# Kernel optimization log

Measured on AMD Instinct MI355X. Metric: run time of the kernel, lower is better.

The kernel has to match this reference:

```python
import jax, jax.numpy as jnp
import numpy as np


def setup_inputs() -> dict:
    key = jax.random.key(0)
    k1, k2, k3, k4 = jax.random.split(key, 4)
    Nq, Nk, D = 8192, 8192, 256
    xq = jax.random.normal(k1, (Nq, D), dtype=jnp.float32)
    xk = jax.random.normal(k2, (Nk, D), dtype=jnp.float32)
    Wq = jax.random.normal(k3, (D, D), dtype=jnp.float32)
    Wk = jax.random.normal(k4, (D, D), dtype=jnp.float32)
    return {"xq": xq, "xk": xk, "Wq": Wq, "Wk": Wk}


def reference(xq, xk, Wq, Wk):
    # Q: [Nq, D], K: [Nk, D]
    Q = xq @ Wq
    K = xk @ Wk
    # scores: [Nq, Nk], consumed only by row-wise logsumexp
    scores = Q @ K.T
    # energy: -sum_i logsumexp_j(scores[i, j])
    return -jnp.sum(jax.nn.logsumexp(scores, axis=1))
```

## Files before the change

### kernel.cpp

```cpp
#include <hip/hip_runtime.h>

typedef unsigned short ushort_t;
typedef __attribute__((ext_vector_type(8))) __bf16 bf16x8;
typedef __attribute__((ext_vector_type(4))) float f32x4;
typedef __attribute__((ext_vector_type(4))) unsigned int u32x4;
typedef __attribute__((ext_vector_type(8))) unsigned short u16x8;

#define NQ 8192
#define NK 8192
#define DD 256
#define NSPLIT 8
#define SEG (NK / NSPLIT)
#define KBLK 64
#define NT (SEG / KBLK)
#define LOG2E 1.4426950408889634f
#define LN2 0.6931471805599453f

using gptr_t = const __attribute__((address_space(1))) void*;
using lptr_t = __attribute__((address_space(3))) void*;

__device__ __forceinline__ float fexp2(float x) { return __builtin_amdgcn_exp2f(x); }
__device__ __forceinline__ float flog2(float x) { return __builtin_amdgcn_logf(x); }

__device__ __forceinline__ ushort_t f2bf(float f) {
  unsigned int u = __builtin_bit_cast(unsigned int, f);
  unsigned int r = 0x7FFFu + ((u >> 16) & 1u);
  return (ushort_t)((u + r) >> 16);
}

__global__ __launch_bounds__(256) void proj_kernel(
    const float* __restrict__ xq, const float* __restrict__ xk,
    const float* __restrict__ Wq, const float* __restrict__ Wk,
    ushort_t* __restrict__ Qb, ushort_t* __restrict__ Kb) {
  __shared__ __align__(16) char wt_lds[64 * 512];
  const float* X = (blockIdx.y == 0) ? xq : xk;
  const float* W = (blockIdx.y == 0) ? Wq : Wk;
  ushort_t* OUT = (blockIdx.y == 0) ? Qb : Kb;
  const float scale = (blockIdx.y == 0) ? LOG2E : 1.0f;

  const int tid = threadIdx.x;
  const int w = tid >> 6, lane = tid & 63;
  const int g = lane >> 4, c = lane & 15;
  const int rbase = blockIdx.x * 64 + w * 16;
  const int ctbase = blockIdx.z * 4;

  {
    const int n_ = tid & 63;
    const int kb = (tid >> 6) * 2;
    const int nglob = blockIdx.z * 64 + n_;
#pragma unroll
    for (int i = 0; i < 32; ++i) {
      int k = i * 8 + kb;
      float w0 = W[(size_t)k * 256 + nglob];
      float w1 = W[(size_t)(k + 1) * 256 + nglob];
      unsigned int pk = (unsigned int)f2bf(w0) | ((unsigned int)f2bf(w1) << 16);
      int ch = i ^ (n_ & 7);
      *reinterpret_cast<unsigned int*>(&wt_lds[n_ * 512 + ch * 16 + (k & 7) * 2]) = pk;
    }
  }

  bf16x8 a[8];
#pragma unroll
  for (int kk = 0; kk < 8; ++kk) {
    const f32x4* px =
        reinterpret_cast<const f32x4*>(X + (size_t)(rbase + c) * DD + kk * 32 + g * 8);
    f32x4 x0 = px[0], x1 = px[1];
    u16x8 v;
#pragma unroll
    for (int j = 0; j < 4; ++j) { v[j] = f2bf(x0[j]); v[4 + j] = f2bf(x1[j]); }
    a[kk] = __builtin_bit_cast(bf16x8, v);
  }
  __syncthreads();

#pragma unroll
  for (int ct0 = 0; ct0 < 4; ++ct0) {
    const int jrl = ct0 * 16 + c;
    f32x4 acc = {0.f, 0.f, 0.f, 0.f};
#pragma unroll
    for (int kk = 0; kk < 8; ++kk) {
      int ch = (kk * 4 + g) ^ (c & 7);
      bf16x8 b = *reinterpret_cast<const bf16x8*>(&wt_lds[jrl * 512 + ch * 16]);
      acc = __builtin_amdgcn_mfma_f32_16x16x32_bf16(a[kk], b, acc, 0, 0, 0);
    }
    int ct = ctbase + ct0;
#pragma unroll
    for (int r = 0; r < 4; ++r)
      OUT[(size_t)(rbase + g * 4 + r) * DD + ct * 16 + c] = f2bf(acc[r] * scale);
  }
}

__global__ __launch_bounds__(256, 2) void scores_lse_kernel(
    const ushort_t* __restrict__ Qb, const ushort_t* __restrict__ Kb,
    float* __restrict__ pm, float* __restrict__ ps) {
  __shared__ __align__(128) char smem[2][KBLK * 512];
  const int tid = threadIdx.x;
  const int w = tid >> 6, lane = tid & 63;
  const int g = lane >> 4, c = lane & 15;
  const int qw = blockIdx.x * 128 + w * 32;
  const int j0 = blockIdx.y * SEG;

  bf16x8 a[2][8];
#pragma unroll
  for (int rt = 0; rt < 2; ++rt)
#pragma unroll
    for (int kk = 0; kk < 8; ++kk) {
      u32x4 v = *reinterpret_cast<const u32x4*>(
          Qb + (size_t)(qw + rt * 16 + c) * DD + kk * 32 + g * 8);
      a[rt][kk] = __builtin_bit_cast(bf16x8, v);
    }
  asm volatile("s_waitcnt vmcnt(0)" ::: "memory");

  const int c2 = (c >> 2) & 1;
  const int lbase = c * 512 + ((g ^ (c & 3)) << 4);
  const int base_e = lbase + c2 * 64;
  const int base_o = lbase - c2 * 64;

  float m[2][4], s[2][4];
#pragma unroll
  for (int rt = 0; rt < 2; ++rt)
#pragma unroll
    for (int r = 0; r < 4; ++r) { m[rt][r] = -3.4e38f; s[rt][r] = 0.f; }

  f32x4 accA[2][4], accB[2][4];

#define STAGE(buf, t)                                                          \
  do {                                                                         \
    const char* kbase_ = (const char*)(Kb + (size_t)(j0 + (t) * KBLK) * DD);   \
    _Pragma("unroll") for (int i_ = 0; i_ < 8; ++i_) {                         \
      int L_ = (w * 8 + i_) * 64 + lane;                                       \
      int row_ = L_ >> 5, ch_ = L_ & 31;                                       \
      const char* src_ = kbase_ + row_ * 512 + ((ch_ ^ (row_ & 7)) * 16);      \
      char* dst_ = &smem[buf][L_ * 16];                                        \
      __builtin_amdgcn_global_load_lds((gptr_t)src_, (lptr_t)dst_, 16, 0, 0);  \
    }                                                                          \
  } while (0)

#define MFMA_TILE(buf, C)                                                      \
  do {                                                                         \
    const char* se_ = &smem[buf][0] + base_e;                                  \
    const char* so_ = &smem[buf][0] + base_o;                                  \
    _Pragma("unroll") for (int rt_ = 0; rt_ < 2; ++rt_)                        \
    _Pragma("unroll") for (int jt_ = 0; jt_ < 4; ++jt_)                        \
        C[rt_][jt_] = (f32x4){0.f, 0.f, 0.f, 0.f};                             \
    __builtin_amdgcn_s_setprio(1);                                             \
    _Pragma("unroll") for (int kk_ = 0; kk_ < 8; kk_ += 2) {                   \
      _Pragma("unroll") for (int jt_ = 0; jt_ < 4; ++jt_) {                    \
        bf16x8 be_ = *reinterpret_cast<const bf16x8*>(se_ + jt_ * 8192 + kk_ * 64); \
        bf16x8 bo_ = *reinterpret_cast<const bf16x8*>(so_ + jt_ * 8192 + (kk_ + 1) * 64); \
        C[0][jt_] = __builtin_amdgcn_mfma_f32_16x16x32_bf16(a[0][kk_], be_, C[0][jt_], 0, 0, 0); \
        C[1][jt_] = __builtin_amdgcn_mfma_f32_16x16x32_bf16(a[1][kk_], be_, C[1][jt_], 0, 0, 0); \
        C[0][jt_] = __builtin_amdgcn_mfma_f32_16x16x32_bf16(a[0][kk_ + 1], bo_, C[0][jt_], 0, 0, 0); \
        C[1][jt_] = __builtin_amdgcn_mfma_f32_16x16x32_bf16(a[1][kk_ + 1], bo_, C[1][jt_], 0, 0, 0); \
      }                                                                        \
    }                                                                          \
    __builtin_amdgcn_s_setprio(0);                                             \
  } while (0)

#define FOLD(F)                                                                \
  do {                                                                         \
    _Pragma("unroll") for (int rt_ = 0; rt_ < 2; ++rt_)                        \
    _Pragma("unroll") for (int r_ = 0; r_ < 4; ++r_) {                         \
      float v0_ = F[rt_][0][r_], v1_ = F[rt_][1][r_];                          \
      float v2_ = F[rt_][2][r_], v3_ = F[rt_][3][r_];                          \
      float tm_ = fmaxf(fmaxf(v0_, v1_), fmaxf(v2_, v3_));                     \
      float mo_ = m[rt_][r_];                                                  \
      float mn_ = fmaxf(mo_, tm_);                                             \
      float sc_ = fexp2(mo_ - mn_);                                            \
      s[rt_][r_] = s[rt_][r_] * sc_ +                                          \
                   (fexp2(v0_ - mn_) + fexp2(v1_ - mn_) +                      \
                    fexp2(v2_ - mn_) + fexp2(v3_ - mn_));                      \
      m[rt_][r_] = mn_;                                                        \
    }                                                                          \
  } while (0)

  STAGE(0, 0);
  STAGE(1, 1);
  asm volatile("s_waitcnt vmcnt(8)" ::: "memory");
  __builtin_amdgcn_s_barrier();
  MFMA_TILE(0, accA);
  asm volatile("s_waitcnt lgkmcnt(0)" ::: "memory");
  __builtin_amdgcn_s_barrier();

#pragma unroll 1
  for (int tt = 1; tt + 1 < NT; tt += 2) {
    STAGE(0, tt + 1);
    FOLD(accA);
    asm volatile("s_waitcnt vmcnt(8)" ::: "memory");
    __builtin_amdgcn_s_barrier();
    MFMA_TILE(1, accB);
    asm volatile("s_waitcnt lgkmcnt(0)" ::: "memory");
    __builtin_amdgcn_s_barrier();

    STAGE(1, tt + 2);
    FOLD(accB);
    asm volatile("s_waitcnt vmcnt(8)" ::: "memory");
    __builtin_amdgcn_s_barrier();
    MFMA_TILE(0, accA);
    asm volatile("s_waitcnt lgkmcnt(0)" ::: "memory");
    __builtin_amdgcn_s_barrier();
  }

  FOLD(accA);
  asm volatile("s_waitcnt vmcnt(0)" ::: "memory");
  __builtin_amdgcn_s_barrier();
  MFMA_TILE(1, accB);
  FOLD(accB);
#undef STAGE
#undef MFMA_TILE
#undef FOLD

#pragma unroll
  for (int rt = 0; rt < 2; ++rt)
#pragma unroll
    for (int r = 0; r < 4; ++r) {
      float M = m[rt][r], S = s[rt][r];
#pragma unroll
      for (int off = 1; off < 16; off <<= 1) {
        float Mo = __shfl_xor(M, off);
        float So = __shfl_xor(S, off);
        float Mn = fmaxf(M, Mo);
        S = S * fexp2(M - Mn) + So * fexp2(Mo - Mn);
        M = Mn;
      }
      if (c == 0) {
        int row = qw + rt * 16 + g * 4 + r;
        pm[blockIdx.y * NQ + row] = M;
        ps[blockIdx.y * NQ + row] = S;
      }
    }
}

__global__ __launch_bounds__(128) void finalize1_kernel(
    const float* __restrict__ pm, const float* __restrict__ ps,
    float* __restrict__ part) {
  const int tid = threadIdx.x;
  const int row = blockIdx.x * 128 + tid;
  float M = -3.4e38f;
#pragma unroll
  for (int k = 0; k < NSPLIT; ++k) M = fmaxf(M, pm[k * NQ + row]);
  float S = 0.f;
#pragma unroll
  for (int k = 0; k < NSPLIT; ++k) S += ps[k * NQ + row] * fexp2(pm[k * NQ + row] - M);
  float v = LN2 * (M + flog2(S));

  __shared__ float red[128];
  red[tid] = v;
  __syncthreads();
#pragma unroll
  for (int st = 64; st > 0; st >>= 1) {
    if (tid < st) red[tid] += red[tid + st];
    __syncthreads();
  }
  if (tid == 0) part[blockIdx.x] = red[0];
}

__global__ __launch_bounds__(64) void finalize2_kernel(
    const float* __restrict__ part, float* __restrict__ out) {
  const int lane = threadIdx.x;
  float v = part[lane];
#pragma unroll
  for (int off = 1; off < 64; off <<= 1) v += __shfl_xor(v, off);
  if (lane == 0) out[0] = -v;
}

extern "C" void kernel_launch(void* const* d_in, const int* in_sizes, int n_in,
                              void* d_out, int out_size, void* d_ws, size_t ws_size,
                              hipStream_t stream) {
  const float* xq = (const float*)d_in[0];
  const float* xk = (const float*)d_in[1];
  const float* Wq = (const float*)d_in[2];
  const float* Wk = (const float*)d_in[3];

  char* ws = (char*)d_ws;
  ushort_t* Qb = (ushort_t*)(ws);
  ushort_t* Kb = (ushort_t*)(ws + (size_t)NQ * DD * 2);
  float* pm = (float*)(ws + (size_t)(NQ + NK) * DD * 2);
  float* ps = pm + (size_t)NSPLIT * NQ;
  float* part = ps + (size_t)NSPLIT * NQ;

  hipLaunchKernelGGL(proj_kernel, dim3(128, 2, 4), dim3(256), 0, stream,
                     xq, xk, Wq, Wk, Qb, Kb);
  hipLaunchKernelGGL(scores_lse_kernel, dim3(NQ / 128, NSPLIT), dim3(256), 0, stream,
                     Qb, Kb, pm, ps);
  hipLaunchKernelGGL(finalize1_kernel, dim3(64), dim3(128), 0, stream, pm, ps, part);
  hipLaunchKernelGGL(finalize2_kernel, dim3(1), dim3(64), 0, stream, part, (float*)d_out);
}
```

Before: 62.21 us.

## Interleave K-tile prefetch with per-column-tile LDS reads and MFMA phases

Restructures the main loop from a two-accumulator ping-pong, where FOLD overlapped with the next tile's MFMAs, into a single accumulator with four phases per K tile. Each phase reads one column sub-tile from LDS, issues a quarter of the next tile's global-to-LDS prefetch, then runs its MFMAs. The aim is to spread memory traffic more evenly across compute and cut register use. In exchange it adds many more barriers per tile and the softmax fold no longer overlaps with MFMA work.

```diff
diff --git a/kernel.cpp b/kernel.cpp
--- a/kernel.cpp
+++ b/kernel.cpp
@@ -121,12 +121,12 @@
 #pragma unroll
     for (int r = 0; r < 4; ++r) { m[rt][r] = -3.4e38f; s[rt][r] = 0.f; }
 
-  f32x4 accA[2][4], accB[2][4];
-
-#define STAGE(buf, t)                                                          \
+  f32x4 acc[2][4];
+
+#define STAGE2(buf, t, p)                                                      \
   do {                                                                         \
     const char* kbase_ = (const char*)(Kb + (size_t)(j0 + (t) * KBLK) * DD);   \
-    _Pragma("unroll") for (int i_ = 0; i_ < 8; ++i_) {                         \
+    _Pragma("unroll") for (int i_ = (p) * 2; i_ < (p) * 2 + 2; ++i_) {         \
       int L_ = (w * 8 + i_) * 64 + lane;                                       \
       int row_ = L_ >> 5, ch_ = L_ & 31;                                       \
       const char* src_ = kbase_ + row_ * 512 + ((ch_ ^ (row_ & 7)) * 16);      \
@@ -135,79 +135,88 @@
     }                                                                          \
   } while (0)
 
-#define MFMA_TILE(buf, C)                                                      \
+#define DSREAD_Q(buf, jt, bq)                                                  \
   do {                                                                         \
-    const char* se_ = &smem[buf][0] + base_e;                                  \
-    const char* so_ = &smem[buf][0] + base_o;                                  \
-    _Pragma("unroll") for (int rt_ = 0; rt_ < 2; ++rt_)                        \
-    _Pragma("unroll") for (int jt_ = 0; jt_ < 4; ++jt_)                        \
-        C[rt_][jt_] = (f32x4){0.f, 0.f, 0.f, 0.f};                             \
+    const char* se_ = &smem[buf][0] + base_e + (jt) * 8192;                    \
+    const char* so_ = &smem[buf][0] + base_o + (jt) * 8192;                    \
+    bq[0] = *reinterpret_cast<const bf16x8*>(se_ + 0 * 64);                    \
+    bq[1] = *reinterpret_cast<const bf16x8*>(so_ + 1 * 64);                    \
+    bq[2] = *reinterpret_cast<const bf16x8*>(se_ + 2 * 64);                    \
+    bq[3] = *reinterpret_cast<const bf16x8*>(so_ + 3 * 64);                    \
+    bq[4] = *reinterpret_cast<const bf16x8*>(se_ + 4 * 64);                    \
+    bq[5] = *reinterpret_cast<const bf16x8*>(so_ + 5 * 64);                    \
+    bq[6] = *reinterpret_cast<const bf16x8*>(se_ + 6 * 64);                    \
+    bq[7] = *reinterpret_cast<const bf16x8*>(so_ + 7 * 64);                    \
+  } while (0)
+
+#define MFMA_Q(jt, bq)                                                         \
+  do {                                                                         \
     __builtin_amdgcn_s_setprio(1);                                             \
-    _Pragma("unroll") for (int kk_ = 0; kk_ < 8; kk_ += 2) {                   \
-      _Pragma("unroll") for (int jt_ = 0; jt_ < 4; ++jt_) {                    \
-        bf16x8 be_ = *reinterpret_cast<const bf16x8*>(se_ + jt_ * 8192 + kk_ * 64); \
-        bf16x8 bo_ = *reinterpret_cast<const bf16x8*>(so_ + jt_ * 8192 + (kk_ + 1) * 64); \
-        C[0][jt_] = __builtin_amdgcn_mfma_f32_16x16x32_bf16(a[0][kk_], be_, C[0][jt_], 0, 0, 0); \
-        C[1][jt_] = __builtin_amdgcn_mfma_f32_16x16x32_bf16(a[1][kk_], be_, C[1][jt_], 0, 0, 0); \
-        C[0][jt_] = __builtin_amdgcn_mfma_f32_16x16x32_bf16(a[0][kk_ + 1], bo_, C[0][jt_], 0, 0, 0); \
-        C[1][jt_] = __builtin_amdgcn_mfma_f32_16x16x32_bf16(a[1][kk_ + 1], bo_, C[1][jt_], 0, 0, 0); \
-      }                                                                        \
+    _Pragma("unroll") for (int kk_ = 0; kk_ < 8; ++kk_) {                      \
+      acc[0][jt] = __builtin_amdgcn_mfma_f32_16x16x32_bf16(a[0][kk_], bq[kk_], acc[0][jt], 0, 0, 0); \
+      acc[1][jt] = __builtin_amdgcn_mfma_f32_16x16x32_bf16(a[1][kk_], bq[kk_], acc[1][jt], 0, 0, 0); \
     }                                                                          \
     __builtin_amdgcn_s_setprio(0);                                             \
   } while (0)
 
-#define FOLD(F)                                                                \
-  do {                                                                         \
-    _Pragma("unroll") for (int rt_ = 0; rt_ < 2; ++rt_)                        \
-    _Pragma("unroll") for (int r_ = 0; r_ < 4; ++r_) {                         \
-      float v0_ = F[rt_][0][r_], v1_ = F[rt_][1][r_];                          \
-      float v2_ = F[rt_][2][r_], v3_ = F[rt_][3][r_];                          \
-      float tm_ = fmaxf(fmaxf(v0_, v1_), fmaxf(v2_, v3_));                     \
-      float mo_ = m[rt_][r_];                                                  \
-      float mn_ = fmaxf(mo_, tm_);                                             \
-      float sc_ = fexp2(mo_ - mn_);                                            \
-      s[rt_][r_] = s[rt_][r_] * sc_ +                                          \
-                   (fexp2(v0_ - mn_) + fexp2(v1_ - mn_) +                      \
-                    fexp2(v2_ - mn_) + fexp2(v3_ - mn_));                      \
-      m[rt_][r_] = mn_;                                                        \
-    }                                                                          \
-  } while (0)
-
-  STAGE(0, 0);
-  STAGE(1, 1);
-  asm volatile("s_waitcnt vmcnt(8)" ::: "memory");
-  __builtin_amdgcn_s_barrier();
-  MFMA_TILE(0, accA);
-  asm volatile("s_waitcnt lgkmcnt(0)" ::: "memory");
-  __builtin_amdgcn_s_barrier();
+  STAGE2(0, 0, 0);
+  STAGE2(0, 0, 1);
+  STAGE2(0, 0, 2);
+  STAGE2(0, 0, 3);
 
 #pragma unroll 1
-  for (int tt = 1; tt + 1 < NT; tt += 2) {
-    STAGE(0, tt + 1);
-    FOLD(accA);
-    asm volatile("s_waitcnt vmcnt(8)" ::: "memory");
-    __builtin_amdgcn_s_barrier();
-    MFMA_TILE(1, accB);
-    asm volatile("s_waitcnt lgkmcnt(0)" ::: "memory");
-    __builtin_amdgcn_s_barrier();
-
-    STAGE(1, tt + 2);
-    FOLD(accB);
-    asm volatile("s_waitcnt vmcnt(8)" ::: "memory");
-    __builtin_amdgcn_s_barrier();
-    MFMA_TILE(0, accA);
-    asm volatile("s_waitcnt lgkmcnt(0)" ::: "memory");
-    __builtin_amdgcn_s_barrier();
-  }
-
-  FOLD(accA);
-  asm volatile("s_waitcnt vmcnt(0)" ::: "memory");
-  __builtin_amdgcn_s_barrier();
-  MFMA_TILE(1, accB);
-  FOLD(accB);
-#undef STAGE
-#undef MFMA_TILE
-#undef FOLD
+  for (int t = 0; t < NT; ++t) {
+    const int cur = t & 1;
+    const bool pf = (t + 1 < NT);
+
+#pragma unroll
+    for (int rt = 0; rt < 2; ++rt)
+#pragma unroll
+      for (int jt = 0; jt < 4; ++jt) acc[rt][jt] = (f32x4){0.f, 0.f, 0.f, 0.f};
+
+    {
+      if (pf) {
+        STAGE2(cur ^ 1, t + 1, 0);
+        asm volatile("s_waitcnt vmcnt(2)" ::: "memory");
+      } else {
+        asm volatile("s_waitcnt vmcnt(0)" ::: "memory");
+      }
+      __builtin_amdgcn_s_barrier();
+      bf16x8 bq[8];
+      DSREAD_Q(cur, 0, bq);
+      asm volatile("s_waitcnt lgkmcnt(0)" ::: "memory");
+      MFMA_Q(0, bq);
+      __builtin_amdgcn_s_barrier();
+    }
+#pragma unroll
+    for (int jt = 1; jt < 4; ++jt) {
+      bf16x8 bq[8];
+      DSREAD_Q(cur, jt, bq);
+      if (pf) STAGE2(cur ^ 1, t + 1, jt);
+      __builtin_amdgcn_s_barrier();
+      asm volatile("s_waitcnt lgkmcnt(0)" ::: "memory");
+      MFMA_Q(jt, bq);
+      __builtin_amdgcn_s_barrier();
+    }
+
+#pragma unroll
+    for (int rt = 0; rt < 2; ++rt)
+#pragma unroll
+      for (int r = 0; r < 4; ++r) {
+        float v0 = acc[rt][0][r], v1 = acc[rt][1][r];
+        float v2 = acc[rt][2][r], v3 = acc[rt][3][r];
+        float tm = fmaxf(fmaxf(v0, v1), fmaxf(v2, v3));
+        float mo = m[rt][r];
+        float mn = fmaxf(mo, tm);
+        float sc = fexp2(mo - mn);
+        s[rt][r] = s[rt][r] * sc +
+                   (fexp2(v0 - mn) + fexp2(v1 - mn) + fexp2(v2 - mn) + fexp2(v3 - mn));
+        m[rt][r] = mn;
+      }
+  }
+#undef STAGE2
+#undef DSREAD_Q
+#undef MFMA_Q
 
 #pragma unroll
   for (int rt = 0; rt < 2; ++rt)
```

New measurement: 62.71 us. No clear change (+0.8%).
